# Performance work log

Hardware: AMD Instinct MI355X
Metric: run time of the kernel (lower is better)

Reference implementation:

```python
import jax, jax.numpy as jnp
import numpy as np

B, N, C, H = 2, 384, 256, 4
D = C // H


def setup_inputs() -> dict:
    key = jax.random.key(0)
    k1, k2 = jax.random.split(key)
    x = jax.random.normal(k1, (B, N, C), dtype=jnp.float32)
    # nn.Linear(dim, 8*dim, bias=False) weight, scaled like default torch init magnitude
    W = jax.random.normal(k2, (8 * C, C), dtype=jnp.float32) / np.float32(np.sqrt(C))
    return {"x": x, "W": W}


def reference(x, W):
    Bx, Nx, Cx = x.shape
    Hh = H
    Dd = Cx // Hh
    scale = Dd ** -0.5
    # w(x): [B,N,8C] -> [B,N,8,H,D] -> [8,B,H,N,D]
    w = (x @ W.T).reshape(Bx, Nx, 8, Hh, Dd).transpose(2, 0, 3, 1, 4)
    a, b, c = w[0], w[1], w[2]          # w[3..5] (d,e,f) are unused in the torch forward
    v1, v2 = w[6], w[7]
    # pairwise logits, each [B,H,N,N]
    eAB = jnp.exp(jnp.einsum('bhid,bhjd->bhij', a, b) * scale)  # indexed [i,j]
    eCD = jnp.exp(jnp.einsum('bhid,bhjd->bhij', b, c) * scale)  # indexed [i,k]
    eEF = jnp.exp(jnp.einsum('bhid,bhjd->bhij', c, a) * scale)  # indexed [j,k]
    # exact factorization of exp(AB[ij]+CD[ik]+EF[jk]):
    # num[i,d] = sum_j eAB[ij] v1[jd] * (sum_k eCD[ik] eEF[jk] v2[kd])
    T = eEF[..., None] * v2[:, :, None, :, :]                   # [B,H,j,k,D]
    R = jnp.einsum('bhik,bhjkd->bhijd', eCD, T)                 # [B,H,i,j,D]
    num = jnp.einsum('bhij,bhjd,bhijd->bhid', eAB, v1, R)       # [B,H,N,D]
    den = jnp.sum(eAB * jnp.einsum('bhik,bhjk->bhij', eCD, eEF), axis=-1)  # [B,H,N]
    out = num / den[..., None]
    # [B,H,N,D] -> [B,N,H,D] -> [B,N,C]
    return out.transpose(0, 2, 1, 3).reshape(Bx, Nx, Cx)
```

## Files before the change

kernel.cpp:

```cpp
#include <hip/hip_runtime.h>
#include <math.h>

#define B_  2
#define N_  384
#define C_  256
#define H_  4
#define D_  64
#define NBH (B_*H_)
#define TSZ (NBH*N_*D_)
#define ESZ (NBH*N_*N_)
#define SCALE 0.125f
#define PIT 72

typedef _Float16 f16;
typedef f16  f16x8 __attribute__((ext_vector_type(8)));
typedef f16  f16x4 __attribute__((ext_vector_type(4)));
typedef float f32x4 __attribute__((ext_vector_type(4)));

__global__ __launch_bounds__(256) void proj_kernel(const float* __restrict__ x,
                                                   const float* __restrict__ W,
                                                   float* __restrict__ proj) {
    __shared__ float Xs[32][68];
    __shared__ float Ws[32][68];
    const int tid = threadIdx.x;
    const int tx = tid & 15, ty = tid >> 4;
    const int m0 = blockIdx.x * 64;
    const int c0 = blockIdx.y * 64;
    const int t  = c0 >> 8;
    const int wbase = ((t >= 3) ? (t + 3) : t) * 256;

    float acc[4][4] = {{0.f}};
    for (int k0 = 0; k0 < 256; k0 += 32) {
        __syncthreads();
#pragma unroll
        for (int l = 0; l < 8; ++l) {
            const int idx = l * 256 + tid;
            const int mi = idx >> 5, kk = idx & 31;
            Xs[kk][mi] = x[(m0 + mi) * 256 + k0 + kk];
            const int rem = (c0 + mi) & 255;
            Ws[kk][mi] = W[(wbase + rem) * 256 + k0 + kk];
        }
        __syncthreads();
#pragma unroll
        for (int kk = 0; kk < 32; ++kk) {
            const float4 xf = *(const float4*)&Xs[kk][ty * 4];
            const float4 wf = *(const float4*)&Ws[kk][tx * 4];
            const float xa[4] = {xf.x, xf.y, xf.z, xf.w};
            const float wa[4] = {wf.x, wf.y, wf.z, wf.w};
#pragma unroll
            for (int q = 0; q < 4; ++q)
#pragma unroll
                for (int p = 0; p < 4; ++p)
                    acc[q][p] += xa[q] * wa[p];
        }
    }
#pragma unroll
    for (int q = 0; q < 4; ++q) {
        const int r = m0 + ty * 4 + q;
        const int b = r / N_;
        const int n = r - b * N_;
#pragma unroll
        for (int p = 0; p < 4; ++p) {
            const int rem = (c0 + tx * 4 + p) & 255;
            const int h = rem >> 6, d = rem & 63;
            proj[t * TSZ + ((b * H_ + h) * N_ + n) * D_ + d] = acc[q][p];
        }
    }
}

__global__ __launch_bounds__(256) void logits_kernel(const float* __restrict__ proj,
                                                     f16* __restrict__ eabt16,
                                                     float* __restrict__ ecd,
                                                     f16* __restrict__ eef16) {
    __shared__ float Xs[32][68];
    __shared__ float Ys[32][68];
    const int tid = threadIdx.x;
    const int tx = tid & 15, ty = tid >> 4;
    const int i0 = blockIdx.x * 64, j0 = blockIdx.y * 64;
    const int q  = blockIdx.z >> 3;
    const int bh = blockIdx.z & 7;
    const int xt = q;
    const int yt = (q == 2) ? 0 : (q + 1);
    const float* Xp = proj + xt * TSZ + bh * N_ * D_;
    const float* Yp = proj + yt * TSZ + bh * N_ * D_;

    float acc[4][4] = {{0.f}};
    for (int k0 = 0; k0 < 64; k0 += 32) {
        __syncthreads();
#pragma unroll
        for (int l = 0; l < 8; ++l) {
            const int idx = l * 256 + tid;
            const int mi = idx >> 5, kk = idx & 31;
            Xs[kk][mi] = Xp[(i0 + mi) * 64 + k0 + kk];
            Ys[kk][mi] = Yp[(j0 + mi) * 64 + k0 + kk];
        }
        __syncthreads();
#pragma unroll
        for (int kk = 0; kk < 32; ++kk) {
            const float4 xf = *(const float4*)&Xs[kk][ty * 4];
            const float4 yf = *(const float4*)&Ys[kk][tx * 4];
            const float xa[4] = {xf.x, xf.y, xf.z, xf.w};
            const float ya[4] = {yf.x, yf.y, yf.z, yf.w};
#pragma unroll
            for (int qq = 0; qq < 4; ++qq)
#pragma unroll
                for (int p = 0; p < 4; ++p)
                    acc[qq][p] += xa[qq] * ya[p];
        }
    }
#pragma unroll
    for (int qq = 0; qq < 4; ++qq)
#pragma unroll
        for (int p = 0; p < 4; ++p) {
            const float e = expf(acc[qq][p] * SCALE);
            const int ii = i0 + ty * 4 + qq;
            const int jj = j0 + tx * 4 + p;
            if (q == 0)      eabt16[(size_t)bh * N_ * N_ + jj * N_ + ii] = (f16)e;
            else if (q == 1) ecd   [(size_t)bh * N_ * N_ + ii * N_ + jj] = e;
            else             eef16 [(size_t)bh * N_ * N_ + ii * N_ + jj] = (f16)e;
        }
}

__global__ __launch_bounds__(256) void triplet_mfma_kernel(
        const f16*  __restrict__ eabt,
        const float* __restrict__ ecd,
        const f16*  __restrict__ eef,
        const float* __restrict__ v1,
        const float* __restrict__ v2,
        float* __restrict__ numout) {
    __shared__ __align__(16) unsigned char smem_raw[62464];
    f16*   us   = (f16*)smem_raw;
    f16*   es   = us + 4 * 64 * PIT;
    f16*   abts = es + 64 * PIT;
    float* v1s  = (float*)(smem_raw + 55296);
    float* v2k  = (float*)(smem_raw + 61440);

    const int tid  = threadIdx.x;
    const int lane = tid & 63;
    const int w    = tid >> 6;
    const int quad = lane >> 4;
    const int lr   = lane & 15;
    const int i0 = blockIdx.x * 64;
    const int dg = blockIdx.y;
    const int bh = blockIdx.z;
    const int dd = dg * 4 + w;

    const f16*   eabtb = eabt + (size_t)bh * N_ * N_;
    const float* ecdb  = ecd  + (size_t)bh * N_ * N_;
    const f16*   eefb  = eef  + (size_t)bh * N_ * N_;
    const float* v1b   = v1 + (size_t)bh * N_ * D_;
    const float* v2b   = v2 + (size_t)bh * N_ * D_;

#pragma unroll
    for (int it = 0; it < 6; ++it) {
        const int id = it * 256 + tid;
        const int j = id >> 2, c = id & 3;
        const int d2 = dg * 4 + c;
        v1s[id] = (d2 < 64) ? v1b[j * 64 + d2] : 1.0f;
    }

    float numacc[16];
#pragma unroll
    for (int r = 0; r < 16; ++r) numacc[r] = 0.f;

    for (int kt = 0; kt < 6; ++kt) {
        const int k0 = kt * 64;
        __syncthreads();
        {
            const int c = tid >> 6, k = tid & 63;
            const int d2 = dg * 4 + c;
            v2k[c * 64 + k] = (d2 < 64) ? v2b[(k0 + k) * 64 + d2] : 1.0f;
        }
        __syncthreads();
#pragma unroll
        for (int it = 0; it < 4; ++it) {
            const int row  = it * 16 + (tid >> 4);
            const int kcol = (tid & 15) * 4;
            const float4 c4 = *(const float4*)&ecdb[(i0 + row) * N_ + k0 + kcol];
#pragma unroll
            for (int d = 0; d < 4; ++d) {
                const float4 w4 = *(const float4*)&v2k[d * 64 + kcol];
                union { f16 h[4]; unsigned long long u; } pk;
                pk.h[0] = (f16)(c4.x * w4.x);
                pk.h[1] = (f16)(c4.y * w4.y);
                pk.h[2] = (f16)(c4.z * w4.z);
                pk.h[3] = (f16)(c4.w * w4.w);
                *(unsigned long long*)(us + d * 64 * PIT + row * PIT + kcol) = pk.u;
            }
        }
        __syncthreads();
        f16x8 af[4][2];
#pragma unroll
        for (int isub = 0; isub < 4; ++isub)
#pragma unroll
            for (int ks = 0; ks < 2; ++ks)
                af[isub][ks] = *(const f16x8*)(us + w * 64 * PIT +
                                               (isub * 16 + lr) * PIT + (ks * 4 + quad) * 8);

        for (int jt = 0; jt < 6; ++jt) {
            const int j0 = jt * 64;
            __syncthreads();
#pragma unroll
            for (int it = 0; it < 2; ++it) {
                const int row = it * 32 + (tid >> 3);
                const int blk = tid & 7;
                *(uint4*)(es   + row * PIT + blk * 8) =
                    *(const uint4*)(eefb  + (j0 + row) * N_ + k0 + blk * 8);
                *(uint4*)(abts + row * PIT + blk * 8) =
                    *(const uint4*)(eabtb + (j0 + row) * N_ + i0 + blk * 8);
            }
            __syncthreads();
            f16x8 bf[4][2];
#pragma unroll
            for (int js = 0; js < 4; ++js)
#pragma unroll
                for (int ks = 0; ks < 2; ++ks)
                    bf[js][ks] = *(const f16x8*)(es + (js * 16 + lr) * PIT + (ks * 4 + quad) * 8);
#pragma unroll
            for (int js = 0; js < 4; ++js) {
                const float v1v = v1s[(j0 + js * 16 + lr) * 4 + w];
#pragma unroll
                for (int isub = 0; isub < 4; ++isub) {
                    f32x4 t = {0.f, 0.f, 0.f, 0.f};
                    t = __builtin_amdgcn_mfma_f32_16x16x32_f16(af[isub][0], bf[js][0], t, 0, 0, 0);
                    t = __builtin_amdgcn_mfma_f32_16x16x32_f16(af[isub][1], bf[js][1], t, 0, 0, 0);
                    const f16x4 ab = *(const f16x4*)(abts + (js * 16 + lr) * PIT +
                                                     isub * 16 + quad * 4);
#pragma unroll
                    for (int q = 0; q < 4; ++q)
                        numacc[isub * 4 + q] += (float)ab[q] * (v1v * t[q]);
                }
            }
        }
    }
#pragma unroll
    for (int r = 0; r < 16; ++r) {
        float v = numacc[r];
        v += __shfl_xor(v, 1);
        v += __shfl_xor(v, 2);
        v += __shfl_xor(v, 4);
        v += __shfl_xor(v, 8);
        numacc[r] = v;
    }
    if (lr == 0) {
#pragma unroll
        for (int r = 0; r < 16; ++r) {
            const int i = (r >> 2) * 16 + quad * 4 + (r & 3);
            numout[((size_t)bh * N_ + i0 + i) * 68 + dd] = numacc[r];
        }
    }
}

__global__ __launch_bounds__(256) void finalize_kernel(const float* __restrict__ numw,
                                                       float* __restrict__ out) {
    const int o = blockIdx.x * 256 + threadIdx.x;
    const int b = o / (N_ * C_);
    const int rem = o - b * (N_ * C_);
    const int n = rem >> 8;
    const int cc = rem & 255;
    const int h = cc >> 6, d = cc & 63;
    const float* base = numw + (((size_t)b * H_ + h) * N_ + n) * 68;
    out[o] = base[d] / base[64];
}

extern "C" void kernel_launch(void* const* d_in, const int* in_sizes, int n_in,
                              void* d_out, int out_size, void* d_ws, size_t ws_size,
                              hipStream_t stream) {
    const float* x = (const float*)d_in[0];
    const float* W = (const float*)d_in[1];
    float* ws    = (float*)d_ws;
    float* proj  = ws;
    float* ecd   = ws + 5 * TSZ;
    float* numw  = ecd + ESZ;
    f16*   eabt  = (f16*)(numw + NBH * N_ * 68);
    f16*   eef   = eabt + ESZ;

    proj_kernel<<<dim3(12, 20), 256, 0, stream>>>(x, W, proj);
    logits_kernel<<<dim3(6, 6, 24), 256, 0, stream>>>(proj, eabt, ecd, eef);
    triplet_mfma_kernel<<<dim3(6, 17, 8), 256, 0, stream>>>(
        eabt, ecd, eef, proj + 3 * TSZ, proj + 4 * TSZ, numw);
    finalize_kernel<<<dim3(768), 256, 0, stream>>>(numw, (float*)d_out);
}
```

Measured before the change: 251.2 us.

## Restructure triplet kernel around resident j-tile of eEF with atomic accumulation

The triplet kernel now assigns each block a 64-row j-tile and keeps the full eEF rows for that tile resident in XOR-swizzled shared memory. It loops over all i-tiles, reading eCD straight from global memory as f16 registers and scaling by v2 on the fly. Partial numerators are combined across j-tiles with atomicAdd into a buffer cleared by a new memset. eCD is now stored as f16 instead of f32, which halves its traffic but lowers its precision. This drops the per-k-tile staging and many barriers, at the cost of atomics, an extra memset and uncached global loads of eCD and eAB^T in the inner loop.

```diff
diff --git a/kernel.cpp b/kernel.cpp
--- a/kernel.cpp
+++ b/kernel.cpp
@@ -10,7 +10,6 @@
 #define TSZ (NBH*N_*D_)
 #define ESZ (NBH*N_*N_)
 #define SCALE 0.125f
-#define PIT 72
 
 typedef _Float16 f16;
 typedef f16  f16x8 __attribute__((ext_vector_type(8)));
@@ -70,7 +69,7 @@
 
 __global__ __launch_bounds__(256) void logits_kernel(const float* __restrict__ proj,
                                                      f16* __restrict__ eabt16,
-                                                     float* __restrict__ ecd,
+                                                     f16* __restrict__ ecd16,
                                                      f16* __restrict__ eef16) {
     __shared__ float Xs[32][68];
     __shared__ float Ys[32][68];
@@ -116,137 +115,127 @@
             const int ii = i0 + ty * 4 + qq;
             const int jj = j0 + tx * 4 + p;
             if (q == 0)      eabt16[(size_t)bh * N_ * N_ + jj * N_ + ii] = (f16)e;
-            else if (q == 1) ecd   [(size_t)bh * N_ * N_ + ii * N_ + jj] = e;
+            else if (q == 1) ecd16 [(size_t)bh * N_ * N_ + ii * N_ + jj] = (f16)e;
             else             eef16 [(size_t)bh * N_ * N_ + ii * N_ + jj] = (f16)e;
         }
 }
 
-__global__ __launch_bounds__(256) void triplet_mfma_kernel(
+__global__ __launch_bounds__(256) void triplet_mfma2_kernel(
         const f16*  __restrict__ eabt,
-        const float* __restrict__ ecd,
-        const f16*  __restrict__ eef,
+        const f16*  __restrict__ ecdh,
+        const f16*  __restrict__ eefh,
         const float* __restrict__ v1,
         const float* __restrict__ v2,
         float* __restrict__ numout) {
-    __shared__ __align__(16) unsigned char smem_raw[62464];
-    f16*   us   = (f16*)smem_raw;
-    f16*   es   = us + 4 * 64 * PIT;
-    f16*   abts = es + 64 * PIT;
-    float* v1s  = (float*)(smem_raw + 55296);
-    float* v2k  = (float*)(smem_raw + 61440);
+    __shared__ __align__(16) f16 eefs[64 * 384];
+    __shared__ __align__(16) f16 v2s[4 * 384];
 
     const int tid  = threadIdx.x;
     const int lane = tid & 63;
     const int w    = tid >> 6;
     const int quad = lane >> 4;
     const int lr   = lane & 15;
-    const int i0 = blockIdx.x * 64;
+    const int j0 = blockIdx.x * 64;
     const int dg = blockIdx.y;
     const int bh = blockIdx.z;
     const int dd = dg * 4 + w;
 
     const f16*   eabtb = eabt + (size_t)bh * N_ * N_;
-    const float* ecdb  = ecd  + (size_t)bh * N_ * N_;
-    const f16*   eefb  = eef  + (size_t)bh * N_ * N_;
+    const f16*   ecdb  = ecdh + (size_t)bh * N_ * N_;
+    const f16*   eefb  = eefh + (size_t)bh * N_ * N_;
     const float* v1b   = v1 + (size_t)bh * N_ * D_;
     const float* v2b   = v2 + (size_t)bh * N_ * D_;
 
-#pragma unroll
+    {
+        const int row = tid >> 2;
+#pragma unroll
+        for (int rep = 0; rep < 12; ++rep) {
+            const int kb = (tid & 3) + rep * 4;
+            *(uint4*)(eefs + row * 384 + ((kb ^ (row & 7)) << 3)) =
+                *(const uint4*)(eefb + (j0 + row) * N_ + kb * 8);
+        }
+    }
+#pragma unroll
+    for (int rep = 0; rep < 6; ++rep) {
+        const int id = rep * 256 + tid;
+        const int c = id / 384, k = id - c * 384;
+        const int d2 = dg * 4 + c;
+        v2s[c * 384 + k] = (f16)((d2 < 64) ? v2b[k * 64 + d2] : 1.0f);
+    }
+    float v1r[4];
+#pragma unroll
+    for (int js = 0; js < 4; ++js)
+        v1r[js] = (dd < 64) ? v1b[(j0 + js * 16 + lr) * 64 + dd] : 1.0f;
+    __syncthreads();
+
+    const int swzbase = lr & 7;
+
     for (int it = 0; it < 6; ++it) {
-        const int id = it * 256 + tid;
-        const int j = id >> 2, c = id & 3;
-        const int d2 = dg * 4 + c;
-        v1s[id] = (d2 < 64) ? v1b[j * 64 + d2] : 1.0f;
-    }
-
-    float numacc[16];
-#pragma unroll
-    for (int r = 0; r < 16; ++r) numacc[r] = 0.f;
-
-    for (int kt = 0; kt < 6; ++kt) {
-        const int k0 = kt * 64;
-        __syncthreads();
-        {
-            const int c = tid >> 6, k = tid & 63;
-            const int d2 = dg * 4 + c;
-            v2k[c * 64 + k] = (d2 < 64) ? v2b[(k0 + k) * 64 + d2] : 1.0f;
-        }
-        __syncthreads();
-#pragma unroll
-        for (int it = 0; it < 4; ++it) {
-            const int row  = it * 16 + (tid >> 4);
-            const int kcol = (tid & 15) * 4;
-            const float4 c4 = *(const float4*)&ecdb[(i0 + row) * N_ + k0 + kcol];
-#pragma unroll
-            for (int d = 0; d < 4; ++d) {
-                const float4 w4 = *(const float4*)&v2k[d * 64 + kcol];
-                union { f16 h[4]; unsigned long long u; } pk;
-                pk.h[0] = (f16)(c4.x * w4.x);
-                pk.h[1] = (f16)(c4.y * w4.y);
-                pk.h[2] = (f16)(c4.z * w4.z);
-                pk.h[3] = (f16)(c4.w * w4.w);
-                *(unsigned long long*)(us + d * 64 * PIT + row * PIT + kcol) = pk.u;
-            }
-        }
-        __syncthreads();
-        f16x8 af[4][2];
+        const int i0 = it * 64;
+        __syncthreads();
+
+        f32x4 acc[4][4];
+#pragma unroll
+        for (int a = 0; a < 4; ++a)
+#pragma unroll
+            for (int b = 0; b < 4; ++b)
+                acc[a][b] = (f32x4){0.f, 0.f, 0.f, 0.f};
+
+        f16x8 pf[4];
 #pragma unroll
         for (int isub = 0; isub < 4; ++isub)
-#pragma unroll
-            for (int ks = 0; ks < 2; ++ks)
-                af[isub][ks] = *(const f16x8*)(us + w * 64 * PIT +
-                                               (isub * 16 + lr) * PIT + (ks * 4 + quad) * 8);
-
-        for (int jt = 0; jt < 6; ++jt) {
-            const int j0 = jt * 64;
-            __syncthreads();
-#pragma unroll
-            for (int it = 0; it < 2; ++it) {
-                const int row = it * 32 + (tid >> 3);
-                const int blk = tid & 7;
-                *(uint4*)(es   + row * PIT + blk * 8) =
-                    *(const uint4*)(eefb  + (j0 + row) * N_ + k0 + blk * 8);
-                *(uint4*)(abts + row * PIT + blk * 8) =
-                    *(const uint4*)(eabtb + (j0 + row) * N_ + i0 + blk * 8);
-            }
-            __syncthreads();
-            f16x8 bf[4][2];
-#pragma unroll
-            for (int js = 0; js < 4; ++js)
-#pragma unroll
-                for (int ks = 0; ks < 2; ++ks)
-                    bf[js][ks] = *(const f16x8*)(es + (js * 16 + lr) * PIT + (ks * 4 + quad) * 8);
+            pf[isub] = *(const f16x8*)(ecdb + (i0 + isub * 16 + lr) * N_ + quad * 8);
+
+        for (int ks = 0; ks < 12; ++ks) {
+            const f16x8 v2f = *(const f16x8*)(v2s + w * 384 + ks * 32 + quad * 8);
+            f16x8 af[4];
+#pragma unroll
+            for (int isub = 0; isub < 4; ++isub)
+                af[isub] = pf[isub] * v2f;
+            if (ks < 11) {
+#pragma unroll
+                for (int isub = 0; isub < 4; ++isub)
+                    pf[isub] = *(const f16x8*)(ecdb + (i0 + isub * 16 + lr) * N_ +
+                                               (ks + 1) * 32 + quad * 8);
+            }
 #pragma unroll
             for (int js = 0; js < 4; ++js) {
-                const float v1v = v1s[(j0 + js * 16 + lr) * 4 + w];
-#pragma unroll
-                for (int isub = 0; isub < 4; ++isub) {
-                    f32x4 t = {0.f, 0.f, 0.f, 0.f};
-                    t = __builtin_amdgcn_mfma_f32_16x16x32_f16(af[isub][0], bf[js][0], t, 0, 0, 0);
-                    t = __builtin_amdgcn_mfma_f32_16x16x32_f16(af[isub][1], bf[js][1], t, 0, 0, 0);
-                    const f16x4 ab = *(const f16x4*)(abts + (js * 16 + lr) * PIT +
-                                                     isub * 16 + quad * 4);
-#pragma unroll
-                    for (int q = 0; q < 4; ++q)
-                        numacc[isub * 4 + q] += (float)ab[q] * (v1v * t[q]);
-                }
-            }
-        }
-    }
-#pragma unroll
-    for (int r = 0; r < 16; ++r) {
-        float v = numacc[r];
-        v += __shfl_xor(v, 1);
-        v += __shfl_xor(v, 2);
-        v += __shfl_xor(v, 4);
-        v += __shfl_xor(v, 8);
-        numacc[r] = v;
-    }
-    if (lr == 0) {
+                const f16x8 bf = *(const f16x8*)(eefs + (js * 16 + lr) * 384 +
+                                                 (((ks * 4 + quad) ^ swzbase) << 3));
+#pragma unroll
+                for (int isub = 0; isub < 4; ++isub)
+                    acc[isub][js] = __builtin_amdgcn_mfma_f32_16x16x32_f16(
+                        af[isub], bf, acc[isub][js], 0, 0, 0);
+            }
+        }
+        float numacc[16];
+#pragma unroll
+        for (int r = 0; r < 16; ++r) numacc[r] = 0.f;
+#pragma unroll
+        for (int js = 0; js < 4; ++js)
+#pragma unroll
+            for (int isub = 0; isub < 4; ++isub) {
+                const f16x4 ab = *(const f16x4*)(eabtb + (j0 + js * 16 + lr) * N_ +
+                                                 i0 + isub * 16 + quad * 4);
+#pragma unroll
+                for (int q = 0; q < 4; ++q)
+                    numacc[isub * 4 + q] += (float)ab[q] * (v1r[js] * acc[isub][js][q]);
+            }
 #pragma unroll
         for (int r = 0; r < 16; ++r) {
-            const int i = (r >> 2) * 16 + quad * 4 + (r & 3);
-            numout[((size_t)bh * N_ + i0 + i) * 68 + dd] = numacc[r];
+            float v = numacc[r];
+            v += __shfl_xor(v, 1);
+            v += __shfl_xor(v, 2);
+            v += __shfl_xor(v, 4);
+            v += __shfl_xor(v, 8);
+            numacc[r] = v;
+        }
+        if (lr == 0 && dd <= 64) {
+#pragma unroll
+            for (int r = 0; r < 16; ++r) {
+                const int i = i0 + (r >> 2) * 16 + quad * 4 + (r & 3);
+                atomicAdd(&numout[((size_t)bh * N_ + i) * 68 + dd], numacc[r]);
+            }
         }
     }
 }
@@ -270,14 +259,15 @@
     const float* W = (const float*)d_in[1];
     float* ws    = (float*)d_ws;
     float* proj  = ws;
-    float* ecd   = ws + 5 * TSZ;
-    float* numw  = ecd + ESZ;
+    float* numw  = ws + 5 * TSZ;
     f16*   eabt  = (f16*)(numw + NBH * N_ * 68);
-    f16*   eef   = eabt + ESZ;
+    f16*   eefh  = eabt + ESZ;
+    f16*   ecdh  = eefh + ESZ;
 
     proj_kernel<<<dim3(12, 20), 256, 0, stream>>>(x, W, proj);
-    logits_kernel<<<dim3(6, 6, 24), 256, 0, stream>>>(proj, eabt, ecd, eef);
-    triplet_mfma_kernel<<<dim3(6, 17, 8), 256, 0, stream>>>(
-        eabt, ecd, eef, proj + 3 * TSZ, proj + 4 * TSZ, numw);
+    logits_kernel<<<dim3(6, 6, 24), 256, 0, stream>>>(proj, eabt, ecdh, eefh);
+    hipMemsetAsync(numw, 0, (size_t)NBH * N_ * 68 * sizeof(float), stream);
+    triplet_mfma2_kernel<<<dim3(6, 17, 8), 256, 0, stream>>>(
+        eabt, ecdh, eefh, proj + 3 * TSZ, proj + 4 * TSZ, numw);
     finalize_kernel<<<dim3(768), 256, 0, stream>>>(numw, (float*)d_out);
 }
```

After: 289.5 us. 15.2% more time.
